# Optimization experiments

Hardware: AMD Instinct MI355X
Metric: run time of the kernel (lower is better)

The kernel has to match this reference:

```python
import jax, jax.numpy as jnp
import numpy as np

HIDDEN = 2048
HEADS = 16
HEAD_DIM = HIDDEN // HEADS  # 128
ROPE_DIM = 64
LATENT = 512
B, S = 4, 2048


def rotate_half(x):
    x1, x2 = jnp.split(x, 2, axis=-1)
    return jnp.concatenate((-x2, x1), axis=-1)


def setup_inputs() -> dict:
    key = jax.random.key(0)
    ks = jax.random.split(key, 10)
    sc = 0.02
    return {
        "x": jax.random.normal(ks[0], (B, S, HIDDEN), jnp.float32),
        "wq_down": jax.random.normal(ks[1], (HIDDEN, LATENT), jnp.float32) * sc,
        "wq_up": jax.random.normal(ks[2], (LATENT, HIDDEN - ROPE_DIM * HEADS), jnp.float32) * sc,
        "wq_rope": jax.random.normal(ks[3], (LATENT, ROPE_DIM * HEADS), jnp.float32) * sc,
        "wk_rope": jax.random.normal(ks[4], (HIDDEN, ROPE_DIM), jnp.float32) * sc,
        "wkv_down": jax.random.normal(ks[5], (HIDDEN, LATENT), jnp.float32) * sc,
        "wk_up": jax.random.normal(ks[6], (LATENT, HIDDEN - ROPE_DIM * HEADS), jnp.float32) * sc,
        "wv_up": jax.random.normal(ks[7], (LATENT, HIDDEN), jnp.float32) * sc,
        "wo": jax.random.normal(ks[8], (HIDDEN, HIDDEN), jnp.float32) * sc,
        "bo": jnp.zeros((HIDDEN,), jnp.float32),
    }


def reference(x, wq_down, wq_up, wq_rope, wk_rope, wkv_down, wk_up, wv_up, wo, bo):
    b, s, _ = x.shape
    # low-rank query path
    q_lat = x @ wq_down                                   # [B,S,L]
    q_c = (q_lat @ wq_up).reshape(b, s, HEADS, -1)        # [B,S,H,hd-rd]
    q_r = (q_lat @ wq_rope).reshape(b, s, HEADS, ROPE_DIM)
    # rotary embedding (emb = concat(freqs, freqs))
    inv_freq = 1.0 / (10000.0 ** (jnp.arange(0, ROPE_DIM, 2, dtype=jnp.float32) / ROPE_DIM))
    freqs = jnp.arange(s, dtype=jnp.float32)[:, None] * inv_freq[None, :]
    emb = jnp.concatenate((freqs, freqs), axis=-1)        # [S,rd]
    cos = jnp.cos(emb)[None, :, None, :]                  # [1,S,1,rd]
    sin = jnp.sin(emb)[None, :, None, :]
    q_r = q_r * cos + rotate_half(q_r) * sin
    # shared latent KV path
    kv_lat = x @ wkv_down                                 # [B,S,L]
    k_r = (x @ wk_rope).reshape(b, s, 1, ROPE_DIM)        # single shared rope-key head
    k_r = k_r * cos + rotate_half(k_r) * sin
    k_r = jnp.broadcast_to(k_r, (b, s, HEADS, ROPE_DIM))
    k_c = (kv_lat @ wk_up).reshape(b, s, HEADS, -1)
    v = (kv_lat @ wv_up).reshape(b, s, HEADS, HEAD_DIM)
    q = jnp.concatenate([q_c, q_r], axis=-1)              # [B,S,H,hd]
    k = jnp.concatenate([k_c, k_r], axis=-1)
    scores = jnp.einsum("bqhd,bkhd->bhqk", q, k) / np.sqrt(HEAD_DIM).astype(np.float32)
    causal = jnp.triu(jnp.ones((s, s), bool), k=1)        # True above diagonal
    scores = jnp.where(causal[None, None], jnp.float32(-10000.0), scores)
    attn = jax.nn.softmax(scores, axis=-1)
    ctx = jnp.einsum("bhqk,bkhd->bqhd", attn, v).reshape(b, s, HIDDEN)
    return ctx @ wo + bo
```

## Files before the change

kernel.cpp:

```cpp
#include <hip/hip_runtime.h>
#include <hip/hip_bf16.h>


#define BB 4
#define SS 2048
#define HH 16
#define HD 128
#define RD 64
#define LAT 512
#define HID 2048

typedef __attribute__((ext_vector_type(8))) short s8v;
typedef __attribute__((ext_vector_type(4))) float f4v;

__device__ __forceinline__ float b2f(short h){
  union { unsigned u; float f; } v; v.u = ((unsigned)(unsigned short)h) << 16; return v.f;
}
__device__ __forceinline__ short f2b(float f){
  union { float f; unsigned u; } v; v.f = f;
  unsigned r = (v.u + 0x7FFFu + ((v.u >> 16) & 1u)) >> 16;
  return (short)r;
}
__device__ __forceinline__ void gload_lds16(const void* g, void* l){
  __builtin_amdgcn_global_load_lds((const __attribute__((address_space(1))) void*)g,
                                   (__attribute__((address_space(3))) void*)l, 16, 0, 0);
}

__global__ void build_trig(float* __restrict__ ct, float* __restrict__ st){
  int idx = blockIdx.x * 256 + threadIdx.x;
  int s = idx >> 5, j = idx & 31;
  float freq = powf(10000.f, -(float)j * (1.f / 32.f));
  float arg = (float)s * freq;
  float sv, cv;
  sincosf(arg, &sv, &cv);
  ct[idx] = cv; st[idx] = sv;
}

__global__ void cast_x(const float* __restrict__ src, short* __restrict__ dst){
  size_t i = ((size_t)blockIdx.x * 256 + threadIdx.x) * 8;
  float4 a = *(const float4*)(src + i);
  float4 b = *(const float4*)(src + i + 4);
  s8v o;
  o[0]=f2b(a.x); o[1]=f2b(a.y); o[2]=f2b(a.z); o[3]=f2b(a.w);
  o[4]=f2b(b.x); o[5]=f2b(b.y); o[6]=f2b(b.z); o[7]=f2b(b.w);
  *(s8v*)(dst + i) = o;
}

__global__ void transpose_cast(const float* __restrict__ src, short* __restrict__ dst,
                               int R, int C, int ldd){
  __shared__ float t[32][33];
  int c0 = blockIdx.x * 32, r0 = blockIdx.y * 32;
  int tx = threadIdx.x & 31, ty = threadIdx.x >> 5;
  #pragma unroll
  for (int i = 0; i < 4; ++i)
    t[ty + i*8][tx] = src[(size_t)(r0 + ty + i*8) * C + c0 + tx];
  __syncthreads();
  #pragma unroll
  for (int i = 0; i < 4; ++i){
    int c = ty + i*8;
    dst[(size_t)(c0 + c) * ldd + r0 + tx] = f2b(t[tx][c]);
  }
}

template<int F32OUT>
__global__ __launch_bounds__(256)
void gemm_bf16(const short* __restrict__ A, const short* __restrict__ Bt,
               void* __restrict__ Cv, const float* __restrict__ bias,
               int K, int lda, int ldb, int ldc)
{
  __shared__ __align__(16) short As[128 * 64];
  __shared__ __align__(16) short Bs[128 * 64];
  const int tid = threadIdx.x;
  const int wave = tid >> 6, lane = tid & 63, hi = lane >> 4, lo = lane & 15;
  const int m0 = blockIdx.y * 128, n0 = blockIdx.x * 128;
  const int wr = wave >> 1, wc = wave & 1;

  const f4v fz = {0.f, 0.f, 0.f, 0.f};
  f4v acc[4][4];
  #pragma unroll
  for (int i = 0; i < 4; ++i)
    #pragma unroll
    for (int j = 0; j < 4; ++j) acc[i][j] = fz;

  const int srow = tid >> 3;
  const int su = (tid & 7) ^ (srow & 7);
  const short* Ag = A + (size_t)(m0 + srow) * lda + su * 8;
  const short* Bg = Bt + (size_t)(n0 + srow) * ldb + su * 8;
  char* AsB = (char*)As + wave * 1024;
  char* BsB = (char*)Bs + wave * 1024;

  for (int k0 = 0; k0 < K; k0 += 64){
    #pragma unroll
    for (int i = 0; i < 4; ++i){
      gload_lds16(Ag + (size_t)(i * 32) * lda + k0, AsB + i * 4096);
      gload_lds16(Bg + (size_t)(i * 32) * ldb + k0, BsB + i * 4096);
    }
    __syncthreads();
    #pragma unroll
    for (int ks = 0; ks < 2; ++ks){
      s8v af[4], bf[4];
      #pragma unroll
      for (int mi = 0; mi < 4; ++mi){
        int row = wr * 64 + mi * 16 + lo;
        int u = (ks * 4 + hi) ^ (row & 7);
        af[mi] = *(const s8v*)((const char*)As + row * 128 + u * 16);
      }
      #pragma unroll
      for (int ni = 0; ni < 4; ++ni){
        int row = wc * 64 + ni * 16 + lo;
        int u = (ks * 4 + hi) ^ (row & 7);
        bf[ni] = *(const s8v*)((const char*)Bs + row * 128 + u * 16);
      }
      #pragma unroll
      for (int mi = 0; mi < 4; ++mi)
        #pragma unroll
        for (int ni = 0; ni < 4; ++ni)
          acc[mi][ni] = __builtin_amdgcn_mfma_f32_16x16x32_bf16(af[mi], bf[ni], acc[mi][ni], 0, 0, 0);
    }
    __syncthreads();
  }

  #pragma unroll
  for (int mi = 0; mi < 4; ++mi){
    #pragma unroll
    for (int ni = 0; ni < 4; ++ni){
      int col = n0 + wc * 64 + ni * 16 + lo;
      #pragma unroll
      for (int r = 0; r < 4; ++r){
        int row = m0 + wr * 64 + mi * 16 + hi * 4 + r;
        float v = acc[mi][ni][r];
        if (F32OUT) ((float*)Cv)[(size_t)row * ldc + col] = v + bias[col];
        else        ((short*)Cv)[(size_t)row * ldc + col] = f2b(v);
      }
    }
  }
}

__global__ void assemble_qk(const short* __restrict__ qall, const short* __restrict__ kvall,
                            const short* __restrict__ latall,
                            const float* __restrict__ ct, const float* __restrict__ st,
                            short* __restrict__ Qg, short* __restrict__ Kg)
{
  const int s = blockIdx.x, b = blockIdx.y, t = threadIdx.x;
  const int e = t * 8, h = e >> 7, dd = e & 127;
  const size_t row = (size_t)b * SS + s;
  const size_t obase = ((size_t)(b * HH + h) * SS + s) * 128 + dd;
  const float scale = 0.088388347648318447f;
  s8v oq, ok;
  if (dd < 64){
    s8v q = *(const s8v*)(qall + row * 2048 + h * 64 + dd);
    s8v k = *(const s8v*)(kvall + row * 3072 + h * 64 + dd);
    #pragma unroll
    for (int j = 0; j < 8; ++j){ oq[j] = f2b(b2f(q[j]) * scale); ok[j] = k[j]; }
  } else {
    int d0 = dd - 64, j0 = d0 & 31;
    bool lohalf = d0 < 32;
    float sgn = lohalf ? -1.f : 1.f;
    int part = lohalf ? d0 + 32 : d0 - 32;
    s8v qa = *(const s8v*)(qall + row * 2048 + 1024 + h * 64 + d0);
    s8v qb = *(const s8v*)(qall + row * 2048 + 1024 + h * 64 + part);
    s8v ka = *(const s8v*)(latall + row * 1152 + 1024 + d0);
    s8v kb = *(const s8v*)(latall + row * 1152 + 1024 + part);
    const float* cp = ct + s * 32 + j0;
    const float* sp = st + s * 32 + j0;
    #pragma unroll
    for (int j = 0; j < 8; ++j){
      float cv = cp[j], sv = sp[j];
      oq[j] = f2b((b2f(qa[j]) * cv + sgn * b2f(qb[j]) * sv) * scale);
      ok[j] = f2b( b2f(ka[j]) * cv + sgn * b2f(kb[j]) * sv);
    }
  }
  *(s8v*)(Qg + obase) = oq;
  *(s8v*)(Kg + obase) = ok;
}

__global__ void vtrans(const short* __restrict__ kvall, short* __restrict__ Vt){
  __shared__ __align__(16) short vt[64 * 136];
  const int stile = blockIdx.x, h = blockIdx.y, b = blockIdx.z, t = threadIdx.x;
  const size_t base = ((size_t)b * SS + stile * 64) * 3072 + 1024 + (size_t)h * 128;
  #pragma unroll
  for (int i = 0; i < 4; ++i){
    int c = i * 256 + t, r = c >> 4, u = c & 15;
    *(s8v*)(vt + r * 136 + u * 8) = *(const s8v*)(kvall + base + (size_t)r * 3072 + u * 8);
  }
  __syncthreads();
  const size_t ob = (size_t)(b * HH + h) * 128 * SS + stile * 64;
  #pragma unroll
  for (int i = 0; i < 4; ++i){
    int c = i * 256 + t, d = c >> 3, j = (c & 7) * 8;
    s8v o;
    #pragma unroll
    for (int jj = 0; jj < 8; ++jj) o[jj] = vt[(j + jj) * 136 + d];
    *(s8v*)(Vt + ob + (size_t)d * SS + j) = o;
  }
}

__global__ __launch_bounds__(256, 2)
void attn_kernel(const short* __restrict__ Qg, const short* __restrict__ Kg,
                 const short* __restrict__ Vg, short* __restrict__ Ctx)
{
  __shared__ __align__(16) short Kt[64 * 128];
  __shared__ __align__(16) short Vl[128 * 64];
  __shared__ __align__(16) short Pl[4][32 * 72];
  const int tid = threadIdx.x;
  const int wave = tid >> 6, lane = tid & 63, hi = lane >> 4, lo = lane & 15;

  int D = blockIdx.x + 16 * (blockIdx.y + 16 * blockIdx.z);
  int xcd = D & 7, k = D >> 3;
  int grp = xcd + 8 * (k >> 4), i = k & 15;
  int qt = 15 - i, h = grp & 15, b = grp >> 4;

  const int q0w = qt * 128 + wave * 32;
  const size_t bh = (size_t)(b * HH + h);
  const short* Qb = Qg + bh * (size_t)SS * 128;
  const short* Kb = Kg + bh * (size_t)SS * 128;
  const short* Vb = Vg + bh * (size_t)128 * SS;

  s8v qf[2][4];
  #pragma unroll
  for (int qfr = 0; qfr < 2; ++qfr)
    #pragma unroll
    for (int ks = 0; ks < 4; ++ks)
      qf[qfr][ks] = *(const s8v*)(Qb + (size_t)(q0w + qfr * 16 + lo) * 128 + ks * 32 + hi * 8);

  const f4v fz = {0.f, 0.f, 0.f, 0.f};
  f4v o[2][8], o9[2];
  #pragma unroll
  for (int qfr = 0; qfr < 2; ++qfr){
    o9[qfr] = fz;
    #pragma unroll
    for (int n = 0; n < 8; ++n) o[qfr][n] = fz;
  }
  const short onev = (lo == 0) ? (short)0x3F80 : (short)0;
  s8v onef;
  #pragma unroll
  for (int j = 0; j < 8; ++j) onef[j] = onev;

  short* Pw = Pl[wave];
  const int nkt = qt * 2 + 2;
  const int wbase = tid & 192;

  for (int kt = 0; kt < nkt; ++kt){
    #pragma unroll
    for (int it = 0; it < 4; ++it){
      int c = it * 256 + tid;
      int krow = c >> 4, ku = (c & 15) ^ (krow & 7);
      gload_lds16(Kb + (size_t)(kt * 64 + krow) * 128 + ku * 8,
                  (char*)Kt + (it * 256 + wbase) * 16);
      int vrow = c >> 3, vu = (c & 7) ^ (vrow & 7);
      gload_lds16(Vb + (size_t)vrow * SS + kt * 64 + vu * 8,
                  (char*)Vl + (it * 256 + wbase) * 16);
    }
    __syncthreads();

    f4v sf[2][4];
    #pragma unroll
    for (int qfr = 0; qfr < 2; ++qfr)
      #pragma unroll
      for (int sub = 0; sub < 4; ++sub) sf[qfr][sub] = fz;
    __builtin_amdgcn_s_setprio(1);
    #pragma unroll
    for (int sub = 0; sub < 4; ++sub){
      s8v kf[4];
      #pragma unroll
      for (int ks = 0; ks < 4; ++ks){
        int row = sub * 16 + lo;
        int u = (ks * 4 + hi) ^ (row & 7);
        kf[ks] = *(const s8v*)((const char*)Kt + row * 256 + u * 16);
      }
      #pragma unroll
      for (int ks = 0; ks < 4; ++ks){
        sf[0][sub] = __builtin_amdgcn_mfma_f32_16x16x32_bf16(qf[0][ks], kf[ks], sf[0][sub], 0, 0, 0);
        sf[1][sub] = __builtin_amdgcn_mfma_f32_16x16x32_bf16(qf[1][ks], kf[ks], sf[1][sub], 0, 0, 0);
      }
    }
    __builtin_amdgcn_s_setprio(0);

    const bool needmask = (kt * 64 + 63) > q0w;
    #pragma unroll
    for (int qfr = 0; qfr < 2; ++qfr){
      #pragma unroll
      for (int sub = 0; sub < 4; ++sub){
        int kg = kt * 64 + sub * 16 + lo;
        int qg = q0w + qfr * 16 + hi * 4;
        #pragma unroll
        for (int r = 0; r < 4; ++r){
          float s = sf[qfr][sub][r];
          if (needmask && kg > qg + r) s = -1e30f;
          Pw[(qfr * 16 + hi * 4 + r) * 72 + sub * 16 + lo] = f2b(__expf(s));
        }
      }
    }

    __builtin_amdgcn_s_setprio(1);
    #pragma unroll
    for (int kc = 0; kc < 2; ++kc){
      s8v pa0 = *(const s8v*)(Pw + lo * 72 + kc * 32 + hi * 8);
      s8v pa1 = *(const s8v*)(Pw + (16 + lo) * 72 + kc * 32 + hi * 8);
      #pragma unroll
      for (int n = 0; n < 8; ++n){
        int row = n * 16 + lo;
        int u = (kc * 4 + hi) ^ (row & 7);
        s8v vf = *(const s8v*)((const char*)Vl + row * 128 + u * 16);
        o[0][n] = __builtin_amdgcn_mfma_f32_16x16x32_bf16(pa0, vf, o[0][n], 0, 0, 0);
        o[1][n] = __builtin_amdgcn_mfma_f32_16x16x32_bf16(pa1, vf, o[1][n], 0, 0, 0);
      }
      o9[0] = __builtin_amdgcn_mfma_f32_16x16x32_bf16(pa0, onef, o9[0], 0, 0, 0);
      o9[1] = __builtin_amdgcn_mfma_f32_16x16x32_bf16(pa1, onef, o9[1], 0, 0, 0);
    }
    __builtin_amdgcn_s_setprio(0);
    __syncthreads();
  }

  #pragma unroll
  for (int qfr = 0; qfr < 2; ++qfr){
    float inv[4];
    #pragma unroll
    for (int r = 0; r < 4; ++r){
      float ls = __shfl(o9[qfr][r], lane & 48);
      inv[r] = 1.f / ls;
    }
    short* outp = Ctx + (size_t)((size_t)b * SS + q0w + qfr * 16) * 2048 + h * 128;
    #pragma unroll
    for (int n = 0; n < 8; ++n)
      #pragma unroll
      for (int r = 0; r < 4; ++r)
        outp[(size_t)(hi * 4 + r) * 2048 + n * 16 + lo] = f2b(o[qfr][n][r] * inv[r]);
  }
}

extern "C" void kernel_launch(void* const* d_in, const int* in_sizes, int n_in,
                              void* d_out, int out_size, void* d_ws, size_t ws_size,
                              hipStream_t stream)
{
  const float* x        = (const float*)d_in[0];
  const float* wq_down  = (const float*)d_in[1];
  const float* wq_up    = (const float*)d_in[2];
  const float* wq_rope  = (const float*)d_in[3];
  const float* wk_rope  = (const float*)d_in[4];
  const float* wkv_down = (const float*)d_in[5];
  const float* wk_up    = (const float*)d_in[6];
  const float* wv_up    = (const float*)d_in[7];
  const float* wo       = (const float*)d_in[8];
  const float* bo       = (const float*)d_in[9];

  char* ws = (char*)d_ws;
  float* cost = (float*)(ws + 0);
  float* sint = (float*)(ws + 262144);
  short* W1t  = (short*)(ws + 524288);
  short* W2t  = (short*)(ws + 5242880);
  short* W3t  = (short*)(ws + 7340032);
  short* Wot  = (short*)(ws + 10485760);
  short* xb   = (short*)(ws + 18874368);
  short* lat  = (short*)(ws + 52428800);
  short* qall = (short*)(ws + 71303168);
  short* kvall= (short*)(ws + 104857600);
  short* Kg   = (short*)(ws + 155189248);
  short* Vt   = (short*)(ws + 188743680);
  short* Qg = xb;
  short* ctx = qall;

  build_trig<<<256, 256, 0, stream>>>(cost, sint);
  cast_x<<<8192, 256, 0, stream>>>(x, xb);
  transpose_cast<<<dim3(16, 64), 256, 0, stream>>>(wq_down,  W1t,                     2048,  512, 2048);
  transpose_cast<<<dim3(16, 64), 256, 0, stream>>>(wkv_down, W1t + (size_t)512*2048,  2048,  512, 2048);
  transpose_cast<<<dim3( 2, 64), 256, 0, stream>>>(wk_rope,  W1t + (size_t)1024*2048, 2048,   64, 2048);
  hipMemsetAsync(W1t + (size_t)1088*2048, 0, (size_t)64*2048*2, stream);
  transpose_cast<<<dim3(32, 16), 256, 0, stream>>>(wq_up,   W2t,                    512, 1024, 512);
  transpose_cast<<<dim3(32, 16), 256, 0, stream>>>(wq_rope, W2t + (size_t)1024*512, 512, 1024, 512);
  transpose_cast<<<dim3(32, 16), 256, 0, stream>>>(wk_up,   W3t,                    512, 1024, 512);
  transpose_cast<<<dim3(64, 16), 256, 0, stream>>>(wv_up,   W3t + (size_t)1024*512, 512, 2048, 512);
  transpose_cast<<<dim3(64, 64), 256, 0, stream>>>(wo, Wot, 2048, 2048, 2048);

  gemm_bf16<0><<<dim3( 9, 64), 256, 0, stream>>>(xb,        W1t, lat,   nullptr, 2048, 2048, 2048, 1152);
  gemm_bf16<0><<<dim3(16, 64), 256, 0, stream>>>(lat,       W2t, qall,  nullptr,  512, 1152,  512, 2048);
  gemm_bf16<0><<<dim3(24, 64), 256, 0, stream>>>(lat + 512, W3t, kvall, nullptr,  512, 1152,  512, 3072);

  assemble_qk<<<dim3(2048, 4), 256, 0, stream>>>(qall, kvall, lat, cost, sint, Qg, Kg);
  vtrans<<<dim3(32, 16, 4), 256, 0, stream>>>(kvall, Vt);
  attn_kernel<<<dim3(16, 16, 4), 256, 0, stream>>>(Qg, Kg, Vt, ctx);

  gemm_bf16<1><<<dim3(16, 64), 256, 0, stream>>>(ctx, Wot, d_out, bo, 2048, 2048, 2048, 2048);
}
```

Before: 533.7 us.

## Split attention work over eight waves with one 16-row query fragment each

The attention kernel now runs 512-thread blocks, and each of 8 waves handles 16 query rows instead of 4 waves handling 32. This halves per-wave accumulator and Q-fragment registers and raises the launch-bounds occupancy target. It also spreads the K/V tile loads over more threads. In exchange, each K/V fragment read from LDS now feeds only one MFMA instead of two, so LDS read traffic per FLOP doubles, and the larger block synchronizes more waves at each barrier.

```diff
diff --git a/kernel.cpp b/kernel.cpp
--- a/kernel.cpp
+++ b/kernel.cpp
@@ -195,13 +195,13 @@
   }
 }
 
-__global__ __launch_bounds__(256, 2)
+__global__ __launch_bounds__(512, 4)
 void attn_kernel(const short* __restrict__ Qg, const short* __restrict__ Kg,
                  const short* __restrict__ Vg, short* __restrict__ Ctx)
 {
   __shared__ __align__(16) short Kt[64 * 128];
   __shared__ __align__(16) short Vl[128 * 64];
-  __shared__ __align__(16) short Pl[4][32 * 72];
+  __shared__ __align__(16) short Pl[8][16 * 72];
   const int tid = threadIdx.x;
   const int wave = tid >> 6, lane = tid & 63, hi = lane >> 4, lo = lane & 15;
 
@@ -210,27 +210,22 @@
   int grp = xcd + 8 * (k >> 4), i = k & 15;
   int qt = 15 - i, h = grp & 15, b = grp >> 4;
 
-  const int q0w = qt * 128 + wave * 32;
+  const int q0w = qt * 128 + wave * 16;
   const size_t bh = (size_t)(b * HH + h);
   const short* Qb = Qg + bh * (size_t)SS * 128;
   const short* Kb = Kg + bh * (size_t)SS * 128;
   const short* Vb = Vg + bh * (size_t)128 * SS;
 
-  s8v qf[2][4];
-  #pragma unroll
-  for (int qfr = 0; qfr < 2; ++qfr)
-    #pragma unroll
-    for (int ks = 0; ks < 4; ++ks)
-      qf[qfr][ks] = *(const s8v*)(Qb + (size_t)(q0w + qfr * 16 + lo) * 128 + ks * 32 + hi * 8);
+  s8v qf[4];
+  #pragma unroll
+  for (int ks = 0; ks < 4; ++ks)
+    qf[ks] = *(const s8v*)(Qb + (size_t)(q0w + lo) * 128 + ks * 32 + hi * 8);
 
   const f4v fz = {0.f, 0.f, 0.f, 0.f};
-  f4v o[2][8], o9[2];
-  #pragma unroll
-  for (int qfr = 0; qfr < 2; ++qfr){
-    o9[qfr] = fz;
-    #pragma unroll
-    for (int n = 0; n < 8; ++n) o[qfr][n] = fz;
-  }
+  f4v o[8], o9;
+  o9 = fz;
+  #pragma unroll
+  for (int n = 0; n < 8; ++n) o[n] = fz;
   const short onev = (lo == 0) ? (short)0x3F80 : (short)0;
   s8v onef;
   #pragma unroll
@@ -238,95 +233,79 @@
 
   short* Pw = Pl[wave];
   const int nkt = qt * 2 + 2;
-  const int wbase = tid & 192;
+  const int wbase = tid & 448;
 
   for (int kt = 0; kt < nkt; ++kt){
     #pragma unroll
-    for (int it = 0; it < 4; ++it){
-      int c = it * 256 + tid;
+    for (int it = 0; it < 2; ++it){
+      int c = it * 512 + tid;
       int krow = c >> 4, ku = (c & 15) ^ (krow & 7);
       gload_lds16(Kb + (size_t)(kt * 64 + krow) * 128 + ku * 8,
-                  (char*)Kt + (it * 256 + wbase) * 16);
+                  (char*)Kt + (it * 512 + wbase) * 16);
       int vrow = c >> 3, vu = (c & 7) ^ (vrow & 7);
       gload_lds16(Vb + (size_t)vrow * SS + kt * 64 + vu * 8,
-                  (char*)Vl + (it * 256 + wbase) * 16);
+                  (char*)Vl + (it * 512 + wbase) * 16);
     }
     __syncthreads();
 
-    f4v sf[2][4];
-    #pragma unroll
-    for (int qfr = 0; qfr < 2; ++qfr)
-      #pragma unroll
-      for (int sub = 0; sub < 4; ++sub) sf[qfr][sub] = fz;
+    f4v sf[4];
+    #pragma unroll
+    for (int sub = 0; sub < 4; ++sub) sf[sub] = fz;
     __builtin_amdgcn_s_setprio(1);
     #pragma unroll
     for (int sub = 0; sub < 4; ++sub){
-      s8v kf[4];
       #pragma unroll
       for (int ks = 0; ks < 4; ++ks){
         int row = sub * 16 + lo;
         int u = (ks * 4 + hi) ^ (row & 7);
-        kf[ks] = *(const s8v*)((const char*)Kt + row * 256 + u * 16);
-      }
-      #pragma unroll
-      for (int ks = 0; ks < 4; ++ks){
-        sf[0][sub] = __builtin_amdgcn_mfma_f32_16x16x32_bf16(qf[0][ks], kf[ks], sf[0][sub], 0, 0, 0);
-        sf[1][sub] = __builtin_amdgcn_mfma_f32_16x16x32_bf16(qf[1][ks], kf[ks], sf[1][sub], 0, 0, 0);
+        s8v kf = *(const s8v*)((const char*)Kt + row * 256 + u * 16);
+        sf[sub] = __builtin_amdgcn_mfma_f32_16x16x32_bf16(qf[ks], kf, sf[sub], 0, 0, 0);
       }
     }
     __builtin_amdgcn_s_setprio(0);
 
     const bool needmask = (kt * 64 + 63) > q0w;
     #pragma unroll
-    for (int qfr = 0; qfr < 2; ++qfr){
-      #pragma unroll
-      for (int sub = 0; sub < 4; ++sub){
-        int kg = kt * 64 + sub * 16 + lo;
-        int qg = q0w + qfr * 16 + hi * 4;
-        #pragma unroll
-        for (int r = 0; r < 4; ++r){
-          float s = sf[qfr][sub][r];
-          if (needmask && kg > qg + r) s = -1e30f;
-          Pw[(qfr * 16 + hi * 4 + r) * 72 + sub * 16 + lo] = f2b(__expf(s));
-        }
+    for (int sub = 0; sub < 4; ++sub){
+      int kg = kt * 64 + sub * 16 + lo;
+      int qg = q0w + hi * 4;
+      #pragma unroll
+      for (int r = 0; r < 4; ++r){
+        float s = sf[sub][r];
+        if (needmask && kg > qg + r) s = -1e30f;
+        Pw[(hi * 4 + r) * 72 + sub * 16 + lo] = f2b(__expf(s));
       }
     }
 
     __builtin_amdgcn_s_setprio(1);
     #pragma unroll
     for (int kc = 0; kc < 2; ++kc){
-      s8v pa0 = *(const s8v*)(Pw + lo * 72 + kc * 32 + hi * 8);
-      s8v pa1 = *(const s8v*)(Pw + (16 + lo) * 72 + kc * 32 + hi * 8);
+      s8v pa = *(const s8v*)(Pw + lo * 72 + kc * 32 + hi * 8);
       #pragma unroll
       for (int n = 0; n < 8; ++n){
         int row = n * 16 + lo;
         int u = (kc * 4 + hi) ^ (row & 7);
         s8v vf = *(const s8v*)((const char*)Vl + row * 128 + u * 16);
-        o[0][n] = __builtin_amdgcn_mfma_f32_16x16x32_bf16(pa0, vf, o[0][n], 0, 0, 0);
-        o[1][n] = __builtin_amdgcn_mfma_f32_16x16x32_bf16(pa1, vf, o[1][n], 0, 0, 0);
-      }
-      o9[0] = __builtin_amdgcn_mfma_f32_16x16x32_bf16(pa0, onef, o9[0], 0, 0, 0);
-      o9[1] = __builtin_amdgcn_mfma_f32_16x16x32_bf16(pa1, onef, o9[1], 0, 0, 0);
+        o[n] = __builtin_amdgcn_mfma_f32_16x16x32_bf16(pa, vf, o[n], 0, 0, 0);
+      }
+      o9 = __builtin_amdgcn_mfma_f32_16x16x32_bf16(pa, onef, o9, 0, 0, 0);
     }
     __builtin_amdgcn_s_setprio(0);
     __syncthreads();
   }
 
-  #pragma unroll
-  for (int qfr = 0; qfr < 2; ++qfr){
-    float inv[4];
-    #pragma unroll
-    for (int r = 0; r < 4; ++r){
-      float ls = __shfl(o9[qfr][r], lane & 48);
-      inv[r] = 1.f / ls;
-    }
-    short* outp = Ctx + (size_t)((size_t)b * SS + q0w + qfr * 16) * 2048 + h * 128;
-    #pragma unroll
-    for (int n = 0; n < 8; ++n)
-      #pragma unroll
-      for (int r = 0; r < 4; ++r)
-        outp[(size_t)(hi * 4 + r) * 2048 + n * 16 + lo] = f2b(o[qfr][n][r] * inv[r]);
-  }
+  float inv[4];
+  #pragma unroll
+  for (int r = 0; r < 4; ++r){
+    float ls = __shfl(o9[r], lane & 48);
+    inv[r] = 1.f / ls;
+  }
+  short* outp = Ctx + (size_t)((size_t)b * SS + q0w) * 2048 + h * 128;
+  #pragma unroll
+  for (int n = 0; n < 8; ++n)
+    #pragma unroll
+    for (int r = 0; r < 4; ++r)
+      outp[(size_t)(hi * 4 + r) * 2048 + n * 16 + lo] = f2b(o[n][r] * inv[r]);
 }
 
 extern "C" void kernel_launch(void* const* d_in, const int* in_sizes, int n_in,
@@ -378,7 +357,7 @@
 
   assemble_qk<<<dim3(2048, 4), 256, 0, stream>>>(qall, kvall, lat, cost, sint, Qg, Kg);
   vtrans<<<dim3(32, 16, 4), 256, 0, stream>>>(kvall, Vt);
-  attn_kernel<<<dim3(16, 16, 4), 256, 0, stream>>>(Qg, Kg, Vt, ctx);
+  attn_kernel<<<dim3(16, 16, 4), 512, 0, stream>>>(Qg, Kg, Vt, ctx);
 
   gemm_bf16<1><<<dim3(16, 64), 256, 0, stream>>>(ctx, Wot, d_out, bo, 2048, 2048, 2048, 2048);
 }
```

Result: slower. 570.6 us (+6.9%).

## Fuse V transpose into up-projection GEMM epilogue and add XCD tile swizzle

Applied to the files above, without the earlier changes.

Splits the KV up-projection into separate K and V GEMMs. The V GEMM gets a new epilogue mode that writes its output directly in the transposed [b,h,d,s] layout the attention kernel expects, so the separate vtrans kernel and the intermediate kvall round trip go away. All GEMMs also remap block IDs so consecutive blocks are spread across the 8 XCDs, aiming for better L2 locality. The transposed-store epilogue writes 4-element vectors with a large stride, which may coalesce less well than the original stores.

```diff
diff --git a/kernel.cpp b/kernel.cpp
--- a/kernel.cpp
+++ b/kernel.cpp
@@ -11,6 +11,7 @@
 #define HID 2048
 
 typedef __attribute__((ext_vector_type(8))) short s8v;
+typedef __attribute__((ext_vector_type(4))) short s4v;
 typedef __attribute__((ext_vector_type(4))) float f4v;
 
 __device__ __forceinline__ float b2f(short h){
@@ -62,7 +63,7 @@
   }
 }
 
-template<int F32OUT>
+template<int MODE>
 __global__ __launch_bounds__(256)
 void gemm_bf16(const short* __restrict__ A, const short* __restrict__ Bt,
                void* __restrict__ Cv, const float* __restrict__ bias,
@@ -72,7 +73,11 @@
   __shared__ __align__(16) short Bs[128 * 64];
   const int tid = threadIdx.x;
   const int wave = tid >> 6, lane = tid & 63, hi = lane >> 4, lo = lane & 15;
-  const int m0 = blockIdx.y * 128, n0 = blockIdx.x * 128;
+  const int gx = gridDim.x;
+  const int bid = blockIdx.y * gx + blockIdx.x;
+  const int cpx = (gx * gridDim.y) >> 3;
+  const int swz = (bid & 7) * cpx + (bid >> 3);
+  const int m0 = (swz / gx) * 128, n0 = (swz % gx) * 128;
   const int wr = wave >> 1, wc = wave & 1;
 
   const f4v fz = {0.f, 0.f, 0.f, 0.f};
@@ -125,18 +130,28 @@
     #pragma unroll
     for (int ni = 0; ni < 4; ++ni){
       int col = n0 + wc * 64 + ni * 16 + lo;
-      #pragma unroll
-      for (int r = 0; r < 4; ++r){
-        int row = m0 + wr * 64 + mi * 16 + hi * 4 + r;
-        float v = acc[mi][ni][r];
-        if (F32OUT) ((float*)Cv)[(size_t)row * ldc + col] = v + bias[col];
-        else        ((short*)Cv)[(size_t)row * ldc + col] = f2b(v);
-      }
-    }
-  }
-}
-
-__global__ void assemble_qk(const short* __restrict__ qall, const short* __restrict__ kvall,
+      if (MODE == 2){
+        int row0 = m0 + wr * 64 + mi * 16 + hi * 4;
+        int b = row0 >> 11, s = row0 & 2047;
+        int h = col >> 7, d = col & 127;
+        s4v pk;
+        #pragma unroll
+        for (int r = 0; r < 4; ++r) pk[r] = f2b(acc[mi][ni][r]);
+        *(s4v*)((short*)Cv + (((size_t)(b * 16 + h) * 128 + d) << 11) + s) = pk;
+      } else {
+        #pragma unroll
+        for (int r = 0; r < 4; ++r){
+          int row = m0 + wr * 64 + mi * 16 + hi * 4 + r;
+          float v = acc[mi][ni][r];
+          if (MODE == 1) ((float*)Cv)[(size_t)row * ldc + col] = v + bias[col];
+          else           ((short*)Cv)[(size_t)row * ldc + col] = f2b(v);
+        }
+      }
+    }
+  }
+}
+
+__global__ void assemble_qk(const short* __restrict__ qall, const short* __restrict__ kall,
                             const short* __restrict__ latall,
                             const float* __restrict__ ct, const float* __restrict__ st,
                             short* __restrict__ Qg, short* __restrict__ Kg)
@@ -149,7 +164,7 @@
   s8v oq, ok;
   if (dd < 64){
     s8v q = *(const s8v*)(qall + row * 2048 + h * 64 + dd);
-    s8v k = *(const s8v*)(kvall + row * 3072 + h * 64 + dd);
+    s8v k = *(const s8v*)(kall + row * 1024 + h * 64 + dd);
     #pragma unroll
     for (int j = 0; j < 8; ++j){ oq[j] = f2b(b2f(q[j]) * scale); ok[j] = k[j]; }
   } else {
@@ -172,27 +187,6 @@
   }
   *(s8v*)(Qg + obase) = oq;
   *(s8v*)(Kg + obase) = ok;
-}
-
-__global__ void vtrans(const short* __restrict__ kvall, short* __restrict__ Vt){
-  __shared__ __align__(16) short vt[64 * 136];
-  const int stile = blockIdx.x, h = blockIdx.y, b = blockIdx.z, t = threadIdx.x;
-  const size_t base = ((size_t)b * SS + stile * 64) * 3072 + 1024 + (size_t)h * 128;
-  #pragma unroll
-  for (int i = 0; i < 4; ++i){
-    int c = i * 256 + t, r = c >> 4, u = c & 15;
-    *(s8v*)(vt + r * 136 + u * 8) = *(const s8v*)(kvall + base + (size_t)r * 3072 + u * 8);
-  }
-  __syncthreads();
-  const size_t ob = (size_t)(b * HH + h) * 128 * SS + stile * 64;
-  #pragma unroll
-  for (int i = 0; i < 4; ++i){
-    int c = i * 256 + t, d = c >> 3, j = (c & 7) * 8;
-    s8v o;
-    #pragma unroll
-    for (int jj = 0; jj < 8; ++jj) o[jj] = vt[(j + jj) * 136 + d];
-    *(s8v*)(Vt + ob + (size_t)d * SS + j) = o;
-  }
 }
 
 __global__ __launch_bounds__(256, 2)
@@ -349,12 +343,13 @@
   float* sint = (float*)(ws + 262144);
   short* W1t  = (short*)(ws + 524288);
   short* W2t  = (short*)(ws + 5242880);
-  short* W3t  = (short*)(ws + 7340032);
+  short* W3kt = (short*)(ws + 7340032);
+  short* W3vt = (short*)(ws + 8388608);
   short* Wot  = (short*)(ws + 10485760);
   short* xb   = (short*)(ws + 18874368);
   short* lat  = (short*)(ws + 52428800);
   short* qall = (short*)(ws + 71303168);
-  short* kvall= (short*)(ws + 104857600);
+  short* kall = (short*)(ws + 104857600);
   short* Kg   = (short*)(ws + 155189248);
   short* Vt   = (short*)(ws + 188743680);
   short* Qg = xb;
@@ -368,16 +363,16 @@
   hipMemsetAsync(W1t + (size_t)1088*2048, 0, (size_t)64*2048*2, stream);
   transpose_cast<<<dim3(32, 16), 256, 0, stream>>>(wq_up,   W2t,                    512, 1024, 512);
   transpose_cast<<<dim3(32, 16), 256, 0, stream>>>(wq_rope, W2t + (size_t)1024*512, 512, 1024, 512);
-  transpose_cast<<<dim3(32, 16), 256, 0, stream>>>(wk_up,   W3t,                    512, 1024, 512);
-  transpose_cast<<<dim3(64, 16), 256, 0, stream>>>(wv_up,   W3t + (size_t)1024*512, 512, 2048, 512);
+  transpose_cast<<<dim3(32, 16), 256, 0, stream>>>(wk_up,   W3kt,                   512, 1024, 512);
+  transpose_cast<<<dim3(64, 16), 256, 0, stream>>>(wv_up,   W3vt,                   512, 2048, 512);
   transpose_cast<<<dim3(64, 64), 256, 0, stream>>>(wo, Wot, 2048, 2048, 2048);
 
-  gemm_bf16<0><<<dim3( 9, 64), 256, 0, stream>>>(xb,        W1t, lat,   nullptr, 2048, 2048, 2048, 1152);
-  gemm_bf16<0><<<dim3(16, 64), 256, 0, stream>>>(lat,       W2t, qall,  nullptr,  512, 1152,  512, 2048);
-  gemm_bf16<0><<<dim3(24, 64), 256, 0, stream>>>(lat + 512, W3t, kvall, nullptr,  512, 1152,  512, 3072);
-
-  assemble_qk<<<dim3(2048, 4), 256, 0, stream>>>(qall, kvall, lat, cost, sint, Qg, Kg);
-  vtrans<<<dim3(32, 16, 4), 256, 0, stream>>>(kvall, Vt);
+  gemm_bf16<0><<<dim3( 9, 64), 256, 0, stream>>>(xb,        W1t,  lat,   nullptr, 2048, 2048, 2048, 1152);
+  gemm_bf16<0><<<dim3(16, 64), 256, 0, stream>>>(lat,       W2t,  qall,  nullptr,  512, 1152,  512, 2048);
+  gemm_bf16<0><<<dim3( 8, 64), 256, 0, stream>>>(lat + 512, W3kt, kall,  nullptr,  512, 1152,  512, 1024);
+  gemm_bf16<2><<<dim3(16, 64), 256, 0, stream>>>(lat + 512, W3vt, Vt,    nullptr,  512, 1152,  512, 2048);
+
+  assemble_qk<<<dim3(2048, 4), 256, 0, stream>>>(qall, kall, lat, cost, sint, Qg, Kg);
   attn_kernel<<<dim3(16, 16, 4), 256, 0, stream>>>(Qg, Kg, Vt, ctx);
 
   gemm_bf16<1><<<dim3(16, 64), 256, 0, stream>>>(ctx, Wot, d_out, bo, 2048, 2048, 2048, 2048);
```

Result: no change. 529.3 us (-0.8%).
